# Kernel optimization log

Measured on AMD Instinct MI355X. Metric: run time of the kernel, lower is better.

The kernel has to match this reference:

```python
import jax, jax.numpy as jnp
import numpy as np

DIM = 512
HEADS = 8
WS = 8  # window_size


def setup_inputs() -> dict:
    key = jax.random.key(0)
    ks = jax.random.split(key, 7)
    b, c, h, w = 4, DIM, 192, 192
    x = jax.random.normal(ks[0], (b, c, h, w), dtype=jnp.float32)
    # conv1x1 weights are [out, in] matrices (kernel dim squeezed)
    wq = jax.random.normal(ks[1], (DIM, DIM), dtype=jnp.float32) * 0.02
    wk = jax.random.normal(ks[2], (DIM, DIM), dtype=jnp.float32) * 0.02
    wv = jax.random.normal(ks[3], (DIM, DIM), dtype=jnp.float32) * 0.02
    wo = jax.random.normal(ks[4], (DIM, DIM), dtype=jnp.float32) * 0.02
    bo = jax.random.normal(ks[5], (DIM,), dtype=jnp.float32) * 0.02
    # learned per-head additive bias over window tokens (trunc_normal std=0.02)
    beta = jax.random.normal(ks[6], (HEADS, WS * WS, WS * WS), dtype=jnp.float32) * 0.02
    return {"x": x, "wq": wq, "wk": wk, "wv": wv, "wo": wo, "bo": bo, "beta": beta}


def reference(x, wq, wk, wv, wo, bo, beta):
    b, c, h, w = x.shape
    s = WS
    pad_r = (-w) % s
    pad_b = (-h) % s
    x = jnp.pad(x, ((0, 0), (0, 0), (0, pad_b), (0, pad_r)))
    H, W = h + pad_b, w + pad_r
    nh, nw = H // s, W // s
    n = s * s
    head_dim = c // HEADS
    scale = head_dim ** -0.5
    # window partition: (b, c, nh, s, nw, s) -> (b*nh*nw, c, n)
    xw = x.reshape(b, c, nh, s, nw, s).transpose(0, 2, 4, 1, 3, 5).reshape(b * nh * nw, c, n)
    B = xw.shape[0]
    q = jnp.einsum('oc,bcn->bon', wq, xw).reshape(B, HEADS, head_dim, n)
    k = jnp.einsum('oc,bcn->bon', wk, xw).reshape(B, HEADS, head_dim, n)
    v = jnp.einsum('oc,bcn->bon', wv, xw).reshape(B, HEADS, head_dim, n)
    attn = jnp.einsum('bhdn,bhdm->bhnm', q, k) * scale + beta  # [B,H,n,n]
    attn = jax.nn.softmax(attn, axis=-1)
    o = jnp.einsum('bhnm,bhdm->bhdn', attn, v).reshape(B, c, n)
    o = jnp.einsum('oc,bcn->bon', wo, o) + bo[None, :, None]
    # window merge back to image
    out = o.reshape(b, nh, nw, c, s, s).transpose(0, 3, 1, 4, 2, 5).reshape(b, c, H, W)
    return out[:, :, :h, :w]
```

## Files before the change

### kernel.cpp

```cpp
#include <hip/hip_runtime.h>

typedef unsigned short ushort_t;
typedef __attribute__((ext_vector_type(4))) float f32x4;
typedef __attribute__((ext_vector_type(8))) short short8;

__device__ __forceinline__ ushort_t f2bf(float f) {
  union { float f; unsigned u; } v; v.f = f;
  unsigned r = v.u + 0x7fffu + ((v.u >> 16) & 1u);
  return (ushort_t)(r >> 16);
}

__global__ __launch_bounds__(256) void cvt_w_k(const float* __restrict__ wq,
                                               const float* __restrict__ wk,
                                               const float* __restrict__ wv,
                                               const float* __restrict__ wo,
                                               ushort_t* __restrict__ dst) {
  int idx = (blockIdx.x * 256 + threadIdx.x) * 4;
  int m = idx >> 18;
  int off = idx & 0x3ffff;
  const float* s = (m == 0) ? wq : (m == 1) ? wk : (m == 2) ? wv : wo;
  float4 v = *(const float4*)(s + off);
  ushort4 o;
  o.x = f2bf(v.x); o.y = f2bf(v.y); o.z = f2bf(v.z); o.w = f2bf(v.w);
  *(ushort4*)(dst + idx) = o;
}

__global__ __launch_bounds__(256) void xpose_k(const float* __restrict__ x,
                                               ushort_t* __restrict__ xT) {
  __shared__ ushort_t tile[128 * 80];
  int bid = blockIdx.x;
  int win = bid >> 2, kc = bid & 3;
  int b = win / 576, rem = win % 576, wh = rem / 24, ww = rem % 24;
  int tid = threadIdx.x;
  {
    int c_l = tid >> 1, half = tid & 1;
    const float* xb = x + (((b * 512 + kc * 128 + c_l) * 192 + wh * 8) * 192 + ww * 8);
#pragma unroll
    for (int ii = 0; ii < 4; ++ii) {
      int i = half * 4 + ii;
      float4 v0 = *(const float4*)(xb + i * 192);
      float4 v1 = *(const float4*)(xb + i * 192 + 4);
      uint4 u;
      u.x = (unsigned)f2bf(v0.x) | ((unsigned)f2bf(v0.y) << 16);
      u.y = (unsigned)f2bf(v0.z) | ((unsigned)f2bf(v0.w) << 16);
      u.z = (unsigned)f2bf(v1.x) | ((unsigned)f2bf(v1.y) << 16);
      u.w = (unsigned)f2bf(v1.z) | ((unsigned)f2bf(v1.w) << 16);
      *(uint4*)&tile[c_l * 80 + i * 8] = u;
    }
  }
  __syncthreads();
  {
    int tok = tid >> 2, q = tid & 3;
    unsigned w[16];
#pragma unroll
    for (int k = 0; k < 16; ++k) {
      unsigned lo = tile[(q * 32 + 2 * k) * 80 + tok];
      unsigned hi = tile[(q * 32 + 2 * k + 1) * 80 + tok];
      w[k] = lo | (hi << 16);
    }
    ushort_t* d = xT + ((win * 64 + tok) * 512 + kc * 128 + q * 32);
#pragma unroll
    for (int s2 = 0; s2 < 4; ++s2) {
      uint4 u; u.x = w[s2 * 4 + 0]; u.y = w[s2 * 4 + 1]; u.z = w[s2 * 4 + 2]; u.w = w[s2 * 4 + 3];
      *(uint4*)(d + s2 * 8) = u;
    }
  }
}

__global__ __launch_bounds__(512) void qkv_attn_k(const ushort_t* __restrict__ xT,
                                                  const ushort_t* __restrict__ wB,
                                                  const float* __restrict__ beta,
                                                  ushort_t* __restrict__ Og) {
  __shared__ ushort_t xws[64 * 520];
  __shared__ ushort_t qs[2][64 * 72];
  __shared__ ushort_t ks[2][64 * 72];
  __shared__ ushort_t vs[2][64 * 72];
  int win = blockIdx.x;
  int t0 = win * 64;
  int tid = threadIdx.x, lane = tid & 63, wid = tid >> 6;
  int l15 = lane & 15, l4 = lane >> 4;

  {
    int token = tid >> 3, cb = (tid & 7) * 64;
    const uint4* src = (const uint4*)(xT + (size_t)(t0 + token) * 512 + cb);
    uint4* dst = (uint4*)&xws[token * 520 + cb];
#pragma unroll
    for (int s2 = 0; s2 < 8; ++s2) dst[s2] = src[s2];
  }
  __syncthreads();

  const f32x4 z = {0.f, 0.f, 0.f, 0.f};

  for (int hcc = 0; hcc < 4; ++hcc) {
    f32x4 aq[4], ak[4], av[4];
#pragma unroll
    for (int i = 0; i < 4; ++i) { aq[i] = z; ak[i] = z; av[i] = z; }
    int ocol = hcc * 128 + wid * 16 + l15;
    const ushort_t* wqr = wB + (size_t)ocol * 512;
    const ushort_t* wkr = wB + 262144 + (size_t)ocol * 512;
    const ushort_t* wvr = wB + 524288 + (size_t)ocol * 512;
#pragma unroll
    for (int kk = 0; kk < 16; ++kk) {
      int cg = kk * 32 + l4 * 8;
      short8 bq = *(const short8*)(wqr + cg);
      short8 bk = *(const short8*)(wkr + cg);
      short8 bv = *(const short8*)(wvr + cg);
#pragma unroll
      for (int nt = 0; nt < 4; ++nt) {
        short8 a = *(const short8*)&xws[(nt * 16 + l15) * 520 + cg];
        aq[nt] = __builtin_amdgcn_mfma_f32_16x16x32_bf16(a, bq, aq[nt], 0, 0, 0);
        ak[nt] = __builtin_amdgcn_mfma_f32_16x16x32_bf16(a, bk, ak[nt], 0, 0, 0);
        av[nt] = __builtin_amdgcn_mfma_f32_16x16x32_bf16(a, bv, av[nt], 0, 0, 0);
      }
    }
    int hw = wid >> 2;
    int dd = (wid * 16 + l15) & 63;
#pragma unroll
    for (int nt = 0; nt < 4; ++nt) {
#pragma unroll
      for (int r = 0; r < 4; ++r) {
        int n = nt * 16 + l4 * 4 + r;
        qs[hw][n * 72 + dd] = f2bf(aq[nt][r]);
        ks[hw][n * 72 + dd] = f2bf(ak[nt][r]);
      }
      uint2 u;
      u.x = (unsigned)f2bf(av[nt][0]) | ((unsigned)f2bf(av[nt][1]) << 16);
      u.y = (unsigned)f2bf(av[nt][2]) | ((unsigned)f2bf(av[nt][3]) << 16);
      *(uint2*)&vs[hw][dd * 72 + nt * 16 + l4 * 4] = u;
    }
    __syncthreads();

    int hh = wid >> 2, rowg = wid & 3;
    int h = hcc * 2 + hh;
    f32x4 sA[4];
#pragma unroll
    for (int i = 0; i < 4; ++i) sA[i] = z;
#pragma unroll
    for (int kk = 0; kk < 2; ++kk) {
      short8 aF = *(const short8*)&qs[hh][(rowg * 16 + l15) * 72 + kk * 32 + l4 * 8];
#pragma unroll
      for (int mt = 0; mt < 4; ++mt) {
        short8 bF = *(const short8*)&ks[hh][(mt * 16 + l15) * 72 + kk * 32 + l4 * 8];
        sA[mt] = __builtin_amdgcn_mfma_f32_16x16x32_bf16(aF, bF, sA[mt], 0, 0, 0);
      }
    }
    const float* betah = beta + h * 4096;
    float p[4][4];
    float rmax[4] = {-1e30f, -1e30f, -1e30f, -1e30f};
#pragma unroll
    for (int mt = 0; mt < 4; ++mt)
#pragma unroll
      for (int r = 0; r < 4; ++r) {
        int n = rowg * 16 + l4 * 4 + r;
        float val = sA[mt][r] * 0.125f + betah[n * 64 + mt * 16 + l15];
        p[mt][r] = val;
        rmax[r] = fmaxf(rmax[r], val);
      }
#pragma unroll
    for (int m = 1; m <= 8; m <<= 1)
#pragma unroll
      for (int r = 0; r < 4; ++r) rmax[r] = fmaxf(rmax[r], __shfl_xor(rmax[r], m, 64));
    float rsum[4] = {0.f, 0.f, 0.f, 0.f};
#pragma unroll
    for (int mt = 0; mt < 4; ++mt)
#pragma unroll
      for (int r = 0; r < 4; ++r) {
        p[mt][r] = __expf(p[mt][r] - rmax[r]);
        rsum[r] += p[mt][r];
      }
#pragma unroll
    for (int m = 1; m <= 8; m <<= 1)
#pragma unroll
      for (int r = 0; r < 4; ++r) rsum[r] += __shfl_xor(rsum[r], m, 64);
    float rinv[4];
#pragma unroll
    for (int r = 0; r < 4; ++r) rinv[r] = 1.f / rsum[r];
    __syncthreads();
#pragma unroll
    for (int mt = 0; mt < 4; ++mt)
#pragma unroll
      for (int r = 0; r < 4; ++r)
        qs[hh][(rowg * 16 + l4 * 4 + r) * 72 + mt * 16 + l15] = f2bf(p[mt][r] * rinv[r]);
    __syncthreads();

    f32x4 oA[4];
#pragma unroll
    for (int i = 0; i < 4; ++i) oA[i] = z;
#pragma unroll
    for (int kk = 0; kk < 2; ++kk) {
      short8 aF = *(const short8*)&qs[hh][(rowg * 16 + l15) * 72 + kk * 32 + l4 * 8];
#pragma unroll
      for (int dt = 0; dt < 4; ++dt) {
        short8 bF = *(const short8*)&vs[hh][(dt * 16 + l15) * 72 + kk * 32 + l4 * 8];
        oA[dt] = __builtin_amdgcn_mfma_f32_16x16x32_bf16(aF, bF, oA[dt], 0, 0, 0);
      }
    }
#pragma unroll
    for (int dt = 0; dt < 4; ++dt)
#pragma unroll
      for (int r = 0; r < 4; ++r) {
        int n = rowg * 16 + l4 * 4 + r;
        Og[(size_t)(t0 + n) * 512 + h * 64 + dt * 16 + l15] = f2bf(oA[dt][r]);
      }
    __syncthreads();
  }
}

__global__ __launch_bounds__(256) void proj_k(const ushort_t* __restrict__ Og,
                                              const ushort_t* __restrict__ woB,
                                              const float* __restrict__ bo,
                                              float* __restrict__ out) {
  __shared__ ushort_t ows[64 * 136];
  int bid = blockIdx.x;
  int win = bid >> 1, mo = (bid & 1) * 256;
  int b = win / 576, rem = win % 576, wh = rem / 24, ww = rem % 24;
  int tid = threadIdx.x, lane = tid & 63, wid = tid >> 6;
  int l15 = lane & 15, l4 = lane >> 4;
  int t0 = win * 64;
  f32x4 z = {0.f, 0.f, 0.f, 0.f};
  f32x4 acc[4][4];
#pragma unroll
  for (int i = 0; i < 4; ++i)
#pragma unroll
    for (int j = 0; j < 4; ++j) acc[i][j] = z;
  int stok = tid >> 2, sq = tid & 3;
  for (int kcc = 0; kcc < 4; ++kcc) {
    {
      const uint4* src = (const uint4*)(Og + ((t0 + stok) * 512 + kcc * 128 + sq * 32));
      uint4* dstv = (uint4*)&ows[stok * 136 + sq * 32];
#pragma unroll
      for (int s2 = 0; s2 < 4; ++s2) dstv[s2] = src[s2];
    }
    __syncthreads();
#pragma unroll
    for (int kk = 0; kk < 4; ++kk) {
      short8 bF[4];
#pragma unroll
      for (int nt = 0; nt < 4; ++nt)
        bF[nt] = *(const short8*)&ows[(nt * 16 + l15) * 136 + kk * 32 + l4 * 8];
      int cg = kcc * 128 + kk * 32 + l4 * 8;
#pragma unroll
      for (int mt = 0; mt < 4; ++mt) {
        int orow = mo + wid * 64 + mt * 16 + l15;
        short8 aF = *(const short8*)(woB + orow * 512 + cg);
#pragma unroll
        for (int nt = 0; nt < 4; ++nt)
          acc[mt][nt] = __builtin_amdgcn_mfma_f32_16x16x32_bf16(aF, bF[nt], acc[mt][nt], 0, 0, 0);
      }
    }
    __syncthreads();
  }
#pragma unroll
  for (int mt = 0; mt < 4; ++mt) {
#pragma unroll
    for (int r = 0; r < 4; ++r) {
      int o = mo + wid * 64 + mt * 16 + l4 * 4 + r;
      float bias = bo[o];
#pragma unroll
      for (int nt = 0; nt < 4; ++nt) {
        int tok = nt * 16 + l15;
        int i = tok >> 3, j = tok & 7;
        out[((b * 512 + o) * 192 + wh * 8 + i) * 192 + ww * 8 + j] = acc[mt][nt][r] + bias;
      }
    }
  }
}

extern "C" void kernel_launch(void* const* d_in, const int* in_sizes, int n_in,
                              void* d_out, int out_size, void* d_ws, size_t ws_size,
                              hipStream_t stream) {
  const float* x    = (const float*)d_in[0];
  const float* wq   = (const float*)d_in[1];
  const float* wk   = (const float*)d_in[2];
  const float* wv   = (const float*)d_in[3];
  const float* wo   = (const float*)d_in[4];
  const float* bo   = (const float*)d_in[5];
  const float* beta = (const float*)d_in[6];

  ushort_t* wB = (ushort_t*)d_ws;
  ushort_t* Og = (ushort_t*)((char*)d_ws + (size_t)4 * 262144 * 2);
  ushort_t* xT = (ushort_t*)d_out;

  cvt_w_k<<<1024, 256, 0, stream>>>(wq, wk, wv, wo, wB);
  xpose_k<<<2304 * 4, 256, 0, stream>>>(x, xT);
  qkv_attn_k<<<2304, 512, 0, stream>>>(xT, wB, beta, Og);
  proj_k<<<2304 * 2, 256, 0, stream>>>(Og, wB + 3 * 262144, bo, (float*)d_out);
}
```

Baseline: 991.0 us.

## Retile output projection as a shared-memory GEMM and batch QKV weight loads

Replaces the per-window projection kernel with a GEMM over 256-token by 64-output tiles. Both operands are staged in shared memory, blocks are swizzled across output tiles, and results go through a shared-memory transpose so outputs are written with coalesced float4 stores. The QKV stage now prefetches four k-steps of weight fragments at once, and two barriers around the softmax writeback are removed. Buffers move from d_out into workspace, 64-bit indexing is added, and launch bounds request one block per CU. The barrier removal could race if warps share qs rows, and the workspace must be large enough for the new buffers.

```diff
diff --git a/kernel.cpp b/kernel.cpp
--- a/kernel.cpp
+++ b/kernel.cpp
@@ -34,7 +34,7 @@
   int tid = threadIdx.x;
   {
     int c_l = tid >> 1, half = tid & 1;
-    const float* xb = x + (((b * 512 + kc * 128 + c_l) * 192 + wh * 8) * 192 + ww * 8);
+    const float* xb = x + ((((size_t)b * 512 + kc * 128 + c_l) * 192 + wh * 8) * 192 + ww * 8);
 #pragma unroll
     for (int ii = 0; ii < 4; ++ii) {
       int i = half * 4 + ii;
@@ -58,7 +58,7 @@
       unsigned hi = tile[(q * 32 + 2 * k + 1) * 80 + tok];
       w[k] = lo | (hi << 16);
     }
-    ushort_t* d = xT + ((win * 64 + tok) * 512 + kc * 128 + q * 32);
+    ushort_t* d = xT + ((size_t)(win * 64 + tok) * 512 + kc * 128 + q * 32);
 #pragma unroll
     for (int s2 = 0; s2 < 4; ++s2) {
       uint4 u; u.x = w[s2 * 4 + 0]; u.y = w[s2 * 4 + 1]; u.z = w[s2 * 4 + 2]; u.w = w[s2 * 4 + 3];
@@ -67,10 +67,10 @@
   }
 }
 
-__global__ __launch_bounds__(512) void qkv_attn_k(const ushort_t* __restrict__ xT,
-                                                  const ushort_t* __restrict__ wB,
-                                                  const float* __restrict__ beta,
-                                                  ushort_t* __restrict__ Og) {
+__global__ __launch_bounds__(512, 1) void qkv_attn_k(const ushort_t* __restrict__ xT,
+                                                     const ushort_t* __restrict__ wB,
+                                                     const float* __restrict__ beta,
+                                                     ushort_t* __restrict__ O) {
   __shared__ ushort_t xws[64 * 520];
   __shared__ ushort_t qs[2][64 * 72];
   __shared__ ushort_t ks[2][64 * 72];
@@ -96,21 +96,29 @@
 #pragma unroll
     for (int i = 0; i < 4; ++i) { aq[i] = z; ak[i] = z; av[i] = z; }
     int ocol = hcc * 128 + wid * 16 + l15;
-    const ushort_t* wqr = wB + (size_t)ocol * 512;
-    const ushort_t* wkr = wB + 262144 + (size_t)ocol * 512;
-    const ushort_t* wvr = wB + 524288 + (size_t)ocol * 512;
-#pragma unroll
-    for (int kk = 0; kk < 16; ++kk) {
-      int cg = kk * 32 + l4 * 8;
-      short8 bq = *(const short8*)(wqr + cg);
-      short8 bk = *(const short8*)(wkr + cg);
-      short8 bv = *(const short8*)(wvr + cg);
-#pragma unroll
-      for (int nt = 0; nt < 4; ++nt) {
-        short8 a = *(const short8*)&xws[(nt * 16 + l15) * 520 + cg];
-        aq[nt] = __builtin_amdgcn_mfma_f32_16x16x32_bf16(a, bq, aq[nt], 0, 0, 0);
-        ak[nt] = __builtin_amdgcn_mfma_f32_16x16x32_bf16(a, bk, ak[nt], 0, 0, 0);
-        av[nt] = __builtin_amdgcn_mfma_f32_16x16x32_bf16(a, bv, av[nt], 0, 0, 0);
+    const ushort_t* wqr = wB + (size_t)ocol * 512 + l4 * 8;
+    const ushort_t* wkr = wqr + 262144;
+    const ushort_t* wvr = wqr + 524288;
+#pragma unroll
+    for (int bb = 0; bb < 4; ++bb) {
+      short8 bq[4], bk[4], bv[4];
+#pragma unroll
+      for (int j = 0; j < 4; ++j) {
+        int cg = (bb * 4 + j) * 32;
+        bq[j] = *(const short8*)(wqr + cg);
+        bk[j] = *(const short8*)(wkr + cg);
+        bv[j] = *(const short8*)(wvr + cg);
+      }
+#pragma unroll
+      for (int j = 0; j < 4; ++j) {
+        int cg = (bb * 4 + j) * 32 + l4 * 8;
+#pragma unroll
+        for (int nt = 0; nt < 4; ++nt) {
+          short8 a = *(const short8*)&xws[(nt * 16 + l15) * 520 + cg];
+          aq[nt] = __builtin_amdgcn_mfma_f32_16x16x32_bf16(a, bq[j], aq[nt], 0, 0, 0);
+          ak[nt] = __builtin_amdgcn_mfma_f32_16x16x32_bf16(a, bk[j], ak[nt], 0, 0, 0);
+          av[nt] = __builtin_amdgcn_mfma_f32_16x16x32_bf16(a, bv[j], av[nt], 0, 0, 0);
+        }
       }
     }
     int hw = wid >> 2;
@@ -175,13 +183,11 @@
     float rinv[4];
 #pragma unroll
     for (int r = 0; r < 4; ++r) rinv[r] = 1.f / rsum[r];
-    __syncthreads();
 #pragma unroll
     for (int mt = 0; mt < 4; ++mt)
 #pragma unroll
       for (int r = 0; r < 4; ++r)
         qs[hh][(rowg * 16 + l4 * 4 + r) * 72 + mt * 16 + l15] = f2bf(p[mt][r] * rinv[r]);
-    __syncthreads();
 
     f32x4 oA[4];
 #pragma unroll
@@ -200,68 +206,103 @@
 #pragma unroll
       for (int r = 0; r < 4; ++r) {
         int n = rowg * 16 + l4 * 4 + r;
-        Og[(size_t)(t0 + n) * 512 + h * 64 + dt * 16 + l15] = f2bf(oA[dt][r]);
-      }
-    __syncthreads();
-  }
-}
-
-__global__ __launch_bounds__(256) void proj_k(const ushort_t* __restrict__ Og,
-                                              const ushort_t* __restrict__ woB,
-                                              const float* __restrict__ bo,
-                                              float* __restrict__ out) {
-  __shared__ ushort_t ows[64 * 136];
+        O[(size_t)(t0 + n) * 512 + h * 64 + dt * 16 + l15] = f2bf(oA[dt][r]);
+      }
+    __syncthreads();
+  }
+}
+
+__global__ __launch_bounds__(256) void proj_k3(const ushort_t* __restrict__ O,
+                                               const ushort_t* __restrict__ woB,
+                                               const float* __restrict__ bo,
+                                               float* __restrict__ out) {
+  __shared__ __align__(16) char smem_raw[64 * 72 * 2 + 256 * 72 * 2];
+  ushort_t* As = (ushort_t*)smem_raw;
+  ushort_t* Bs = (ushort_t*)smem_raw + 64 * 72;
+  float* Ct = (float*)smem_raw;
   int bid = blockIdx.x;
-  int win = bid >> 1, mo = (bid & 1) * 256;
-  int b = win / 576, rem = win % 576, wh = rem / 24, ww = rem % 24;
+  int cwg = gridDim.x >> 3;
+  int wg = (bid & 7) * cwg + (bid >> 3);
+  int nn = wg >> 3, mm = wg & 7;
   int tid = threadIdx.x, lane = tid & 63, wid = tid >> 6;
   int l15 = lane & 15, l4 = lane >> 4;
-  int t0 = win * 64;
-  f32x4 z = {0.f, 0.f, 0.f, 0.f};
+  const ushort_t* Asrc = woB + (size_t)(mm * 64) * 512;
+  const ushort_t* Bsrc = O + (size_t)(nn * 256) * 512;
+
+  const f32x4 z = {0.f, 0.f, 0.f, 0.f};
   f32x4 acc[4][4];
 #pragma unroll
   for (int i = 0; i < 4; ++i)
 #pragma unroll
     for (int j = 0; j < 4; ++j) acc[i][j] = z;
-  int stok = tid >> 2, sq = tid & 3;
-  for (int kcc = 0; kcc < 4; ++kcc) {
-    {
-      const uint4* src = (const uint4*)(Og + ((t0 + stok) * 512 + kcc * 128 + sq * 32));
-      uint4* dstv = (uint4*)&ows[stok * 136 + sq * 32];
-#pragma unroll
-      for (int s2 = 0; s2 < 4; ++s2) dstv[s2] = src[s2];
-    }
-    __syncthreads();
-#pragma unroll
-    for (int kk = 0; kk < 4; ++kk) {
-      short8 bF[4];
-#pragma unroll
-      for (int nt = 0; nt < 4; ++nt)
-        bF[nt] = *(const short8*)&ows[(nt * 16 + l15) * 136 + kk * 32 + l4 * 8];
-      int cg = kcc * 128 + kk * 32 + l4 * 8;
-#pragma unroll
-      for (int mt = 0; mt < 4; ++mt) {
-        int orow = mo + wid * 64 + mt * 16 + l15;
-        short8 aF = *(const short8*)(woB + orow * 512 + cg);
-#pragma unroll
-        for (int nt = 0; nt < 4; ++nt)
-          acc[mt][nt] = __builtin_amdgcn_mfma_f32_16x16x32_bf16(aF, bF[nt], acc[mt][nt], 0, 0, 0);
-      }
-    }
-    __syncthreads();
-  }
-#pragma unroll
-  for (int mt = 0; mt < 4; ++mt) {
-#pragma unroll
-    for (int r = 0; r < 4; ++r) {
-      int o = mo + wid * 64 + mt * 16 + l4 * 4 + r;
+
+  int arow[2], aslot[2];
+#pragma unroll
+  for (int c = 0; c < 2; ++c) { int u = c * 256 + tid; arow[c] = u >> 3; aslot[c] = u & 7; }
+  int brow[8], bslot[8];
+#pragma unroll
+  for (int c = 0; c < 8; ++c) { int u = c * 256 + tid; brow[c] = u >> 3; bslot[c] = u & 7; }
+
+  for (int ks = 0; ks < 8; ++ks) {
+    int ko = ks * 64;
+    uint4 ta[2], tb[8];
+#pragma unroll
+    for (int c = 0; c < 2; ++c)
+      ta[c] = *(const uint4*)&Asrc[(size_t)arow[c] * 512 + ko + aslot[c] * 8];
+#pragma unroll
+    for (int c = 0; c < 8; ++c)
+      tb[c] = *(const uint4*)&Bsrc[(size_t)brow[c] * 512 + ko + bslot[c] * 8];
+    __syncthreads();
+#pragma unroll
+    for (int c = 0; c < 2; ++c) *(uint4*)&As[arow[c] * 72 + aslot[c] * 8] = ta[c];
+#pragma unroll
+    for (int c = 0; c < 8; ++c) *(uint4*)&Bs[brow[c] * 72 + bslot[c] * 8] = tb[c];
+    __syncthreads();
+#pragma unroll
+    for (int kk = 0; kk < 2; ++kk) {
+      short8 aF[4], bF[4];
+#pragma unroll
+      for (int mi = 0; mi < 4; ++mi)
+        aF[mi] = *(const short8*)&As[(mi * 16 + l15) * 72 + kk * 32 + l4 * 8];
+#pragma unroll
+      for (int ni = 0; ni < 4; ++ni)
+        bF[ni] = *(const short8*)&Bs[(wid * 64 + ni * 16 + l15) * 72 + kk * 32 + l4 * 8];
+#pragma unroll
+      for (int mi = 0; mi < 4; ++mi)
+#pragma unroll
+        for (int ni = 0; ni < 4; ++ni)
+          acc[mi][ni] = __builtin_amdgcn_mfma_f32_16x16x32_bf16(aF[mi], bF[ni], acc[mi][ni], 0, 0, 0);
+    }
+  }
+#pragma unroll
+  for (int p = 0; p < 2; ++p) {
+    __syncthreads();
+#pragma unroll
+    for (int mi = 0; mi < 4; ++mi)
+#pragma unroll
+      for (int nq = 0; nq < 2; ++nq)
+#pragma unroll
+        for (int rr = 0; rr < 4; ++rr) {
+          int o = mi * 16 + l4 * 4 + rr;
+          int i3 = nq * 2 + (l15 >> 3);
+          int col = i3 * 32 + wid * 8 + (l15 & 7);
+          Ct[o * 132 + col] = acc[mi][p * 2 + nq][rr];
+        }
+    __syncthreads();
+#pragma unroll
+    for (int it = 0; it < 8; ++it) {
+      int cidx = it * 256 + tid;
+      int o_l = cidx >> 5, c4 = cidx & 31;
+      float4 v = *(const float4*)&Ct[o_l * 132 + c4 * 4];
+      int o = mm * 64 + o_l;
       float bias = bo[o];
-#pragma unroll
-      for (int nt = 0; nt < 4; ++nt) {
-        int tok = nt * 16 + l15;
-        int i = tok >> 3, j = tok & 7;
-        out[((b * 512 + o) * 192 + wh * 8 + i) * 192 + ww * 8 + j] = acc[mt][nt][r] + bias;
-      }
+      int w = (c4 & 7) >> 1, j = (c4 & 1) * 4, i = p * 4 + (c4 >> 3);
+      int win = nn * 4 + w;
+      int b = win / 576, rem = win % 576, wh = rem / 24, ww = rem % 24;
+      size_t addr = (((size_t)b * 512 + o) * 192 + wh * 8 + i) * 192 + ww * 8 + j;
+      float4 r;
+      r.x = v.x + bias; r.y = v.y + bias; r.z = v.z + bias; r.w = v.w + bias;
+      *(float4*)&out[addr] = r;
     }
   }
 }
@@ -278,11 +319,11 @@
   const float* beta = (const float*)d_in[6];
 
   ushort_t* wB = (ushort_t*)d_ws;
-  ushort_t* Og = (ushort_t*)((char*)d_ws + (size_t)4 * 262144 * 2);
-  ushort_t* xT = (ushort_t*)d_out;
+  ushort_t* xT = (ushort_t*)((char*)d_ws + (size_t)2097152);
+  ushort_t* O  = (ushort_t*)((char*)d_ws + (size_t)2097152 + (size_t)147456 * 1024);
 
   cvt_w_k<<<1024, 256, 0, stream>>>(wq, wk, wv, wo, wB);
   xpose_k<<<2304 * 4, 256, 0, stream>>>(x, xT);
-  qkv_attn_k<<<2304, 512, 0, stream>>>(xT, wB, beta, Og);
-  proj_k<<<2304 * 2, 256, 0, stream>>>(Og, wB + 3 * 262144, bo, (float*)d_out);
-}
+  qkv_attn_k<<<2304, 512, 0, stream>>>(xT, wB, beta, O);
+  proj_k3<<<(147456 / 256) * 8, 256, 0, stream>>>(O, wB + 3 * 262144, bo, (float*)d_out);
+}
```

Result: slower. 1.174 ms (+18.5%).
